# Kernel optimization log

Measured on AMD Instinct MI355X. Metric: run time of the kernel, lower is better.

The kernel has to match this reference:

```python
import jax, jax.numpy as jnp
import numpy as np

SELF_ATTN = -5e4  # reformer TOKEN_SELF_ATTN_VALUE


def _lsh_self_attention(h, w_qk, w_v, w_out, b_out, rotations, n_heads, bucket_size):
    # h: [B, N, D] with N divisible by 2*bucket_size (pre-padded)
    B, N, D = h.shape
    E = D // n_heads
    n_buckets = N // bucket_size
    n_hashes = rotations.shape[1]
    # shared-QK projections, heads merged into batch (batch-major, like reformer)
    qk = (h @ w_qk).reshape(B, N, n_heads, E).transpose(0, 2, 1, 3).reshape(B * n_heads, N, E)
    v = (h @ w_v).reshape(B, N, n_heads, E).transpose(0, 2, 1, 3).reshape(B * n_heads, N, E)
    # --- LSH hashing: argmax over [rot, -rot] ---
    rot = jnp.einsum('bne,ehr->bhnr', qk, rotations)          # [BH, n_hashes, N, n_buckets/2]
    rot = jnp.concatenate([rot, -rot], axis=-1)               # [BH, n_hashes, N, n_buckets]
    buckets = jnp.argmax(rot, axis=-1)                        # [BH, n_hashes, N]
    buckets = buckets + (jnp.arange(n_hashes) * n_buckets)[None, :, None]
    buckets = buckets.reshape(B * n_heads, n_hashes * N)
    # --- sort tokens by (bucket, position) ---
    ticker = jnp.arange(n_hashes * N)
    buckets_and_t = N * buckets + (ticker % N)                # unique keys -> deterministic sort
    sticker = jnp.argsort(buckets_and_t, axis=-1)
    undo = jnp.argsort(sticker, axis=-1)
    st = sticker % N                                          # original positions, sorted order
    sqk = jnp.take_along_axis(qk, st[..., None], axis=1)      # [BH, n_hashes*N, E]
    sv = jnp.take_along_axis(v, st[..., None], axis=1)
    # --- chunk and attend locally (with look-one-back) ---
    nc = n_hashes * n_buckets
    bq = sqk.reshape(-1, nc, bucket_size, E)
    bk = bq / jnp.maximum(jnp.linalg.norm(bq, axis=-1, keepdims=True), 1e-12)  # normalized shared keys
    bv = sv.reshape(-1, nc, bucket_size, E)
    bts = st.reshape(-1, nc, bucket_size)
    look = lambda t: jnp.concatenate([t, jnp.roll(t, 1, axis=1)], axis=2)
    bk, bv, bkt = look(bk), look(bv), look(bts)
    dots = jnp.einsum('bcie,bcje->bcij', bq, bk) * (E ** -0.5)  # [BH, nc, bs, 2*bs]
    dots = jnp.where(bts[..., :, None] == bkt[..., None, :], SELF_ATTN, dots)  # mask self
    lse = jax.scipy.special.logsumexp(dots, axis=-1, keepdims=True)
    p = jnp.exp(dots - lse)
    bo = jnp.einsum('bcij,bcje->bcie', p, bv)
    so = bo.reshape(-1, n_hashes * N, E)
    slog = lse.reshape(-1, n_hashes * N)
    # --- unsort and combine hash rounds by softmax over logsumexp logits ---
    o = jnp.take_along_axis(so, undo[..., None], axis=1).reshape(-1, n_hashes, N, E)
    logits = jnp.take_along_axis(slog, undo, axis=1).reshape(-1, n_hashes, N, 1)
    probs = jnp.exp(logits - jax.scipy.special.logsumexp(logits, axis=1, keepdims=True))
    out = jnp.sum(o * probs, axis=1)                          # [BH, N, E]
    out = out.reshape(B, n_heads, N, E).transpose(0, 2, 1, 3).reshape(B, N, D)
    return out @ w_out + b_out


def setup_inputs() -> dict:
    key = jax.random.key(0)
    ks = jax.random.split(key, 8)
    b, l, n = 16, 12, 325
    d_feat, d_pos, heads, bucket, n_hashes = 256, 64, 8, 16, 4
    pad = 2 * bucket - n % (2 * bucket)
    n_buckets = (n + pad) // bucket
    E = d_feat // heads
    s = 0.05
    return {
        'x': jax.random.normal(ks[0], (b, l, n, d_feat), dtype=jnp.float32),
        'ste': jax.random.normal(ks[1], (b, l, n, d_pos), dtype=jnp.float32),
        'w_proj': jax.random.normal(ks[2], (d_feat + d_pos, d_feat), dtype=jnp.float32) * s,
        'b_proj': jnp.zeros((d_feat,), jnp.float32),
        'w_qk': jax.random.normal(ks[3], (d_feat, d_feat), dtype=jnp.float32) * s,
        'w_v': jax.random.normal(ks[4], (d_feat, d_feat), dtype=jnp.float32) * s,
        'w_out': jax.random.normal(ks[5], (d_feat, d_feat), dtype=jnp.float32) * s,
        'b_out': jnp.zeros((d_feat,), jnp.float32),
        'rotations': jax.random.normal(ks[6], (E, n_hashes, n_buckets // 2), dtype=jnp.float32),
        'n_heads': heads,
        'bucket_size': bucket,
    }


def reference(x, ste, w_proj, b_proj, w_qk, w_v, w_out, b_out, rotations, n_heads, bucket_size):
    b, l, n, d = x.shape
    h = jnp.concatenate([x, ste], axis=-1).reshape(b * l, n, -1)
    h = h @ w_proj + b_proj                                   # projection to d_hidden_feat
    pad = 2 * bucket_size - n % (2 * bucket_size)             # always > 0 (as in the source)
    h = jnp.pad(h, ((0, 0), (0, pad), (0, 0)))
    h = _lsh_self_attention(h, w_qk, w_v, w_out, b_out, rotations, n_heads, bucket_size)
    h = h[:, :-pad, :]
    return h.reshape(b, l, n, -1)
```

## Files before the change

### kernel.cpp

```cpp
#include <hip/hip_runtime.h>
#include <math.h>

#define BL 192
#define NREAL 325
#define NPAD 352
#define DM 256
#define DPOS 64
#define DIN 320
#define NHEADS 8
#define EDIM 32
#define NHASH 4
#define BS 16
#define NBUCK 22
#define NCHUNK 88
#define BHTOT 1536
#define RROT 11
#define W2COLS 352
#define RTM 8
#define HTM 16

__global__ __launch_bounds__(256) void h_kernel(
    const float* __restrict__ x, const float* __restrict__ ste,
    const float* __restrict__ wproj, const float* __restrict__ bproj,
    float* __restrict__ h) {
  int tile = blockIdx.x, bl = blockIdx.y;
  int d = threadIdx.x;
  int n0 = tile * HTM;
  float acc[HTM];
#pragma unroll
  for (int m = 0; m < HTM; ++m) acc[m] = 0.f;
  if (n0 + HTM <= NREAL) {
    const float* xb = x + (size_t)(bl * NREAL + n0) * DM;
    const float* sb = ste + (size_t)(bl * NREAL + n0) * DPOS;
    for (int k = 0; k < DM; k += 4) {
      float b0 = wproj[(k + 0) * DM + d];
      float b1 = wproj[(k + 1) * DM + d];
      float b2 = wproj[(k + 2) * DM + d];
      float b3 = wproj[(k + 3) * DM + d];
#pragma unroll
      for (int m = 0; m < HTM; ++m) {
        const float* xr = xb + (size_t)m * DM + k;
        acc[m] = fmaf(xr[0], b0, acc[m]);
        acc[m] = fmaf(xr[1], b1, acc[m]);
        acc[m] = fmaf(xr[2], b2, acc[m]);
        acc[m] = fmaf(xr[3], b3, acc[m]);
      }
    }
    for (int k = 0; k < DPOS; k += 4) {
      float b0 = wproj[(DM + k + 0) * DM + d];
      float b1 = wproj[(DM + k + 1) * DM + d];
      float b2 = wproj[(DM + k + 2) * DM + d];
      float b3 = wproj[(DM + k + 3) * DM + d];
#pragma unroll
      for (int m = 0; m < HTM; ++m) {
        const float* sr = sb + (size_t)m * DPOS + k;
        acc[m] = fmaf(sr[0], b0, acc[m]);
        acc[m] = fmaf(sr[1], b1, acc[m]);
        acc[m] = fmaf(sr[2], b2, acc[m]);
        acc[m] = fmaf(sr[3], b3, acc[m]);
      }
    }
  } else if (n0 < NREAL) {
#pragma unroll
    for (int m = 0; m < HTM; ++m) {
      if (n0 + m < NREAL) {
        const float* xr = x + (size_t)(bl * NREAL + n0 + m) * DM;
        const float* sr = ste + (size_t)(bl * NREAL + n0 + m) * DPOS;
        for (int k = 0; k < DM; ++k) acc[m] = fmaf(xr[k], wproj[k * DM + d], acc[m]);
        for (int k = 0; k < DPOS; ++k)
          acc[m] = fmaf(sr[k], wproj[(DM + k) * DM + d], acc[m]);
      }
    }
  }
  float bb = bproj[d];
#pragma unroll
  for (int m = 0; m < HTM; ++m) {
    int n = n0 + m;
    h[((size_t)(bl * NPAD + n)) * DM + d] = (n < NREAL) ? (acc[m] + bb) : 0.f;
  }
}

__global__ __launch_bounds__(256) void qkv_rot_bucket_kernel(
    const float* __restrict__ h, const float* __restrict__ wqk,
    const float* __restrict__ wv, const float* __restrict__ rotations,
    int* __restrict__ buckets, float* __restrict__ qk_out,
    float* __restrict__ v_out) {
  int tile = blockIdx.x, bl = blockIdx.y;
  int tid = threadIdx.x;
  __shared__ float Qs[RTM][DM];
  __shared__ float Rs[RTM][W2COLS];
  int n0 = tile * RTM;
  const float* hb = h + (size_t)(bl * NPAD + n0) * DM;
  float aq[RTM], av[RTM];
#pragma unroll
  for (int m = 0; m < RTM; ++m) { aq[m] = 0.f; av[m] = 0.f; }
  for (int k = 0; k < DM; k += 4) {
    float q0 = wqk[(k + 0) * DM + tid];
    float q1 = wqk[(k + 1) * DM + tid];
    float q2 = wqk[(k + 2) * DM + tid];
    float q3 = wqk[(k + 3) * DM + tid];
    float w0 = wv[(k + 0) * DM + tid];
    float w1 = wv[(k + 1) * DM + tid];
    float w2 = wv[(k + 2) * DM + tid];
    float w3 = wv[(k + 3) * DM + tid];
#pragma unroll
    for (int m = 0; m < RTM; ++m) {
      const float* hr = hb + (size_t)m * DM + k;
      float a0 = hr[0], a1 = hr[1], a2 = hr[2], a3 = hr[3];
      aq[m] = fmaf(a0, q0, aq[m]);
      aq[m] = fmaf(a1, q1, aq[m]);
      aq[m] = fmaf(a2, q2, aq[m]);
      aq[m] = fmaf(a3, q3, aq[m]);
      av[m] = fmaf(a0, w0, av[m]);
      av[m] = fmaf(a1, w1, av[m]);
      av[m] = fmaf(a2, w2, av[m]);
      av[m] = fmaf(a3, w3, av[m]);
    }
  }
  {
    int head = tid >> 5, e = tid & 31;
    size_t bh = (size_t)(bl * NHEADS + head);
#pragma unroll
    for (int m = 0; m < RTM; ++m) {
      Qs[m][tid] = aq[m];
      int n = n0 + m;
      qk_out[(bh * NPAD + n) * EDIM + e] = aq[m];
      v_out[(bh * NPAD + n) * EDIM + e] = av[m];
    }
  }
  __syncthreads();
  for (int col = tid; col < W2COLS; col += 256) {
    int head = col / 44;
    int hr = col - head * 44;
    int hs = hr / RROT;
    int r = hr - hs * RROT;
    float acc[RTM];
#pragma unroll
    for (int m = 0; m < RTM; ++m) acc[m] = 0.f;
    {
#pragma clang fp contract(off)
      for (int e = 0; e < EDIM; ++e) {
        float rr = rotations[(e * NHASH + hs) * RROT + r];
#pragma unroll
        for (int m = 0; m < RTM; ++m) {
          float p = Qs[m][head * EDIM + e] * rr;
          acc[m] = acc[m] + p;
        }
      }
    }
#pragma unroll
    for (int m = 0; m < RTM; ++m) Rs[m][col] = acc[m];
  }
  __syncthreads();
  {
    int m = tid >> 5;
    int rest = tid & 31;
    int head = rest >> 2;
    int hs = rest & 3;
    int cbase = head * 44 + hs * RROT;
    float bestv = Rs[m][cbase];
    int best = 0;
    for (int r = 1; r < RROT; ++r) {
      float dv = Rs[m][cbase + r];
      if (dv > bestv) { bestv = dv; best = r; }
    }
    for (int r = 0; r < RROT; ++r) {
      float dv = -Rs[m][cbase + r];
      if (dv > bestv) { bestv = dv; best = RROT + r; }
    }
    int n = n0 + m;
    int bh = bl * NHEADS + head;
    buckets[((size_t)(bh * NHASH + hs)) * NPAD + n] = best;
  }
}

__global__ __launch_bounds__(384) void sort_kernel(const int* __restrict__ buckets,
                                                   int* __restrict__ st) {
  int bh = blockIdx.x, hs = blockIdx.y;
  int n = threadIdx.x;
  __shared__ int buck[NPAD];
  const int* brow = buckets + ((size_t)(bh * NHASH + hs)) * NPAD;
  if (n < NPAD) buck[n] = brow[n];
  __syncthreads();
  if (n < NPAD) {
    int b = buck[n];
    int dest = 0;
    for (int m2 = 0; m2 < NPAD; ++m2) {
      int bm = buck[m2];
      dest += (int)((bm < b) | ((bm == b) & (m2 < n)));
    }
    st[((size_t)(bh * NHASH + hs)) * NPAD + dest] = n;
  }
}

__global__ __launch_bounds__(512) void attn_lse_kernel(
    const float* __restrict__ qk, const int* __restrict__ st,
    float* __restrict__ ll) {
  int c = blockIdx.x, bh = blockIdx.y;
  int t = threadIdx.x;
  int i = t >> 5, j = t & 31;
  __shared__ float qs[16][EDIM];
  __shared__ float ks[32][EDIM + 1];
  __shared__ int qpos[16];
  __shared__ int kpos[32];
  __shared__ float rnorm[32];
  const int* strow = st + (size_t)bh * (NHASH * NPAD);
  int pc = (c + NCHUNK - 1) % NCHUNK;
  if (t < 16) {
    qpos[t] = strow[c * BS + t];
  } else if (t < 48) {
    int jj = t - 16;
    kpos[jj] = (jj < BS) ? strow[c * BS + jj] : strow[pc * BS + (jj - BS)];
  }
  __syncthreads();
  const float* qkb = qk + (size_t)bh * NPAD * EDIM;
  qs[i][j] = qkb[qpos[i] * EDIM + j];
#pragma unroll
  for (int rep = 0; rep < 2; ++rep) {
    int lin = t + rep * 512;
    int r = lin >> 5, cc = lin & 31;
    ks[r][cc] = qkb[kpos[r] * EDIM + cc];
  }
  __syncthreads();
  if (t < 32) {
    float s = 0.f;
#pragma unroll
    for (int e = 0; e < EDIM; ++e) { float kv = ks[t][e]; s = fmaf(kv, kv, s); }
    rnorm[t] = 1.0f / fmaxf(sqrtf(s), 1e-12f);
  }
  __syncthreads();
  float dot = 0.f;
#pragma unroll
  for (int e = 0; e < EDIM; ++e) dot = fmaf(qs[i][e], ks[j][e], dot);
  dot *= rnorm[j] * 0.17677669529663688f;
  if (qpos[i] == kpos[j]) dot = -50000.0f;
  float mx = dot;
#pragma unroll
  for (int off = 16; off > 0; off >>= 1) mx = fmaxf(mx, __shfl_xor(mx, off, 32));
  float ex = expf(dot - mx);
  float sm = ex;
#pragma unroll
  for (int off = 16; off > 0; off >>= 1) sm += __shfl_xor(sm, off, 32);
  if (j == 0) {
    int hs = c / NBUCK;
    ll[((size_t)(bh * NHASH + hs)) * NPAD + qpos[i]] = mx + logf(sm);
  }
}

__global__ __launch_bounds__(256) void lcomb_kernel(const float* __restrict__ ll,
                                                    float* __restrict__ L) {
  int gid = blockIdx.x * 256 + threadIdx.x;
  if (gid >= BHTOT * NPAD) return;
  int n = gid % NPAD, bh = gid / NPAD;
  float l0 = ll[((size_t)(bh * NHASH + 0)) * NPAD + n];
  float l1 = ll[((size_t)(bh * NHASH + 1)) * NPAD + n];
  float l2 = ll[((size_t)(bh * NHASH + 2)) * NPAD + n];
  float l3 = ll[((size_t)(bh * NHASH + 3)) * NPAD + n];
  float m = fmaxf(fmaxf(l0, l1), fmaxf(l2, l3));
  float s = expf(l0 - m) + expf(l1 - m) + expf(l2 - m) + expf(l3 - m);
  L[gid] = m + logf(s);
}

__global__ __launch_bounds__(512) void attn_out_kernel(
    const float* __restrict__ qk, const float* __restrict__ v,
    const int* __restrict__ st, const float* __restrict__ L,
    float* __restrict__ att) {
  int c = blockIdx.x, bh = blockIdx.y;
  int t = threadIdx.x;
  int i = t >> 5, j = t & 31;
  __shared__ float qs[16][EDIM];
  __shared__ float ks[32][EDIM + 1];
  __shared__ float vs[32][EDIM + 1];
  __shared__ float ps[16][32];
  __shared__ int qpos[16];
  __shared__ int kpos[32];
  __shared__ float rnorm[32];
  const int* strow = st + (size_t)bh * (NHASH * NPAD);
  int pc = (c + NCHUNK - 1) % NCHUNK;
  if (t < 16) {
    qpos[t] = strow[c * BS + t];
  } else if (t < 48) {
    int jj = t - 16;
    kpos[jj] = (jj < BS) ? strow[c * BS + jj] : strow[pc * BS + (jj - BS)];
  }
  __syncthreads();
  const float* qkb = qk + (size_t)bh * NPAD * EDIM;
  const float* vb = v + (size_t)bh * NPAD * EDIM;
  qs[i][j] = qkb[qpos[i] * EDIM + j];
#pragma unroll
  for (int rep = 0; rep < 2; ++rep) {
    int lin = t + rep * 512;
    int r = lin >> 5, cc = lin & 31;
    ks[r][cc] = qkb[kpos[r] * EDIM + cc];
    vs[r][cc] = vb[kpos[r] * EDIM + cc];
  }
  __syncthreads();
  if (t < 32) {
    float s = 0.f;
#pragma unroll
    for (int e = 0; e < EDIM; ++e) { float kv = ks[t][e]; s = fmaf(kv, kv, s); }
    rnorm[t] = 1.0f / fmaxf(sqrtf(s), 1e-12f);
  }
  __syncthreads();
  float dot = 0.f;
#pragma unroll
  for (int e = 0; e < EDIM; ++e) dot = fmaf(qs[i][e], ks[j][e], dot);
  dot *= rnorm[j] * 0.17677669529663688f;
  if (qpos[i] == kpos[j]) dot = -50000.0f;
  ps[i][j] = expf(dot - L[(size_t)bh * NPAD + qpos[i]]);
  __syncthreads();
  float acc = 0.f;
#pragma unroll
  for (int jj = 0; jj < 32; ++jj) acc = fmaf(ps[i][jj], vs[jj][j], acc);
  int head = bh & 7, bl = bh >> 3;
  int qp = qpos[i];
  atomicAdd(&att[((size_t)(bl * NPAD + qp)) * DM + head * EDIM + j], acc);
}

__global__ __launch_bounds__(256) void outproj_kernel(
    const float* __restrict__ att, const float* __restrict__ w,
    const float* __restrict__ bias, float* __restrict__ out) {
  int tile = blockIdx.x, bl = blockIdx.y;
  int d = threadIdx.x;
  int n0 = tile * HTM;
  float acc[HTM];
#pragma unroll
  for (int m = 0; m < HTM; ++m) acc[m] = 0.f;
  if (n0 + HTM <= NREAL) {
    const float* ab = att + (size_t)(bl * NPAD + n0) * DM;
    for (int k = 0; k < DM; k += 4) {
      float b0 = w[(k + 0) * DM + d];
      float b1 = w[(k + 1) * DM + d];
      float b2 = w[(k + 2) * DM + d];
      float b3 = w[(k + 3) * DM + d];
#pragma unroll
      for (int m = 0; m < HTM; ++m) {
        const float* ar = ab + (size_t)m * DM + k;
        acc[m] = fmaf(ar[0], b0, acc[m]);
        acc[m] = fmaf(ar[1], b1, acc[m]);
        acc[m] = fmaf(ar[2], b2, acc[m]);
        acc[m] = fmaf(ar[3], b3, acc[m]);
      }
    }
  } else if (n0 < NREAL) {
#pragma unroll
    for (int m = 0; m < HTM; ++m) {
      if (n0 + m < NREAL) {
        const float* ar = att + (size_t)(bl * NPAD + n0 + m) * DM;
        for (int k = 0; k < DM; ++k) acc[m] = fmaf(ar[k], w[k * DM + d], acc[m]);
      }
    }
  } else {
    return;
  }
  float bb = bias[d];
#pragma unroll
  for (int m = 0; m < HTM; ++m) {
    int n = n0 + m;
    if (n < NREAL) out[((size_t)(bl * NREAL + n)) * DM + d] = acc[m] + bb;
  }
}

extern "C" void kernel_launch(void* const* d_in, const int* in_sizes, int n_in,
                              void* d_out, int out_size, void* d_ws, size_t ws_size,
                              hipStream_t stream) {
  (void)in_sizes; (void)n_in; (void)out_size;
  const float* x = (const float*)d_in[0];
  const float* ste = (const float*)d_in[1];
  const float* w_proj = (const float*)d_in[2];
  const float* b_proj = (const float*)d_in[3];
  const float* w_qk = (const float*)d_in[4];
  const float* w_v = (const float*)d_in[5];
  const float* w_out = (const float*)d_in[6];
  const float* b_out = (const float*)d_in[7];
  const float* rotations = (const float*)d_in[8];
  float* out = (float*)d_out;

  const size_t szh = (size_t)BL * NPAD * DM;
  const size_t szst = (size_t)BHTOT * NHASH * NPAD;
  const size_t szL = (size_t)BHTOT * NPAD;
  const size_t needed = 3 * szh * 4 + 2 * szst * 4 + szL * 4;
  if (ws_size < needed) return;

  float* qk = (float*)d_ws;
  float* v = qk + szh;
  float* att = v + szh;
  float* h = att;
  int* st = (int*)(att + szh);
  int* buckets = st + szst;
  float* ll = (float*)buckets;
  float* L = (float*)(buckets + szst);

  h_kernel<<<dim3(NPAD / HTM, BL), dim3(256), 0, stream>>>(
      x, ste, w_proj, b_proj, h);
  qkv_rot_bucket_kernel<<<dim3(NPAD / RTM, BL), dim3(256), 0, stream>>>(
      h, w_qk, w_v, rotations, buckets, qk, v);
  (void)hipMemsetAsync(att, 0, szh * sizeof(float), stream);
  sort_kernel<<<dim3(BHTOT, NHASH), dim3(384), 0, stream>>>(buckets, st);
  attn_lse_kernel<<<dim3(NCHUNK, BHTOT), dim3(512), 0, stream>>>(qk, st, ll);
  lcomb_kernel<<<dim3((BHTOT * NPAD + 255) / 256), dim3(256), 0, stream>>>(ll, L);
  attn_out_kernel<<<dim3(NCHUNK, BHTOT), dim3(512), 0, stream>>>(qk, v, st, L, att);
  outproj_kernel<<<dim3(21, BL), dim3(256), 0, stream>>>(att, w_out, b_out, out);
}
```

Baseline: 1.807 ms.

## Fuse LSH attention LSE, combine and output into one per-head block kernel

Replaces the three attention kernels (per-chunk log-sum-exp, hash combine, output) and the workspace memset with a single kernel that gives each batch-head to one 512-thread block. The block stages all shared-QK rows, key norms and sort indices in LDS once, computes per-hash LSE, combines it across hashes, then recomputes the dots and accumulates outputs into an LDS buffer before writing them out with plain stores. This removes repeated global gathers of q/k/v per chunk, the intermediate ll/L round-trips and the global atomics. In exchange it uses roughly 130KB of LDS per block, which limits occupancy to one block per CU, and it computes the dot products twice.

Result: no change. 1.843 ms (+2.0%).

```diff
diff --git a/kernel.cpp b/kernel.cpp
--- a/kernel.cpp
+++ b/kernel.cpp
@@ -18,6 +18,8 @@
 #define W2COLS 352
 #define RTM 8
 #define HTM 16
+#define QKP 9
+#define OPW 33
 
 __global__ __launch_bounds__(256) void h_kernel(
     const float* __restrict__ x, const float* __restrict__ ste,
@@ -193,128 +195,160 @@
   }
 }
 
-__global__ __launch_bounds__(512) void attn_lse_kernel(
-    const float* __restrict__ qk, const int* __restrict__ st,
-    float* __restrict__ ll) {
-  int c = blockIdx.x, bh = blockIdx.y;
+__global__ __launch_bounds__(512) void attn_fused_kernel(
+    const float* __restrict__ qk, const float* __restrict__ v,
+    const int* __restrict__ st, float* __restrict__ att) {
+  int bh = blockIdx.x;
   int t = threadIdx.x;
-  int i = t >> 5, j = t & 31;
-  __shared__ float qs[16][EDIM];
-  __shared__ float ks[32][EDIM + 1];
-  __shared__ int qpos[16];
-  __shared__ int kpos[32];
-  __shared__ float rnorm[32];
-  const int* strow = st + (size_t)bh * (NHASH * NPAD);
-  int pc = (c + NCHUNK - 1) % NCHUNK;
-  if (t < 16) {
-    qpos[t] = strow[c * BS + t];
-  } else if (t < 48) {
-    int jj = t - 16;
-    kpos[jj] = (jj < BS) ? strow[c * BS + jj] : strow[pc * BS + (jj - BS)];
-  }
-  __syncthreads();
-  const float* qkb = qk + (size_t)bh * NPAD * EDIM;
-  qs[i][j] = qkb[qpos[i] * EDIM + j];
-#pragma unroll
-  for (int rep = 0; rep < 2; ++rep) {
-    int lin = t + rep * 512;
-    int r = lin >> 5, cc = lin & 31;
-    ks[r][cc] = qkb[kpos[r] * EDIM + cc];
-  }
-  __syncthreads();
-  if (t < 32) {
-    float s = 0.f;
-#pragma unroll
-    for (int e = 0; e < EDIM; ++e) { float kv = ks[t][e]; s = fmaf(kv, kv, s); }
-    rnorm[t] = 1.0f / fmaxf(sqrtf(s), 1e-12f);
-  }
-  __syncthreads();
-  float dot = 0.f;
-#pragma unroll
-  for (int e = 0; e < EDIM; ++e) dot = fmaf(qs[i][e], ks[j][e], dot);
-  dot *= rnorm[j] * 0.17677669529663688f;
-  if (qpos[i] == kpos[j]) dot = -50000.0f;
-  float mx = dot;
-#pragma unroll
-  for (int off = 16; off > 0; off >>= 1) mx = fmaxf(mx, __shfl_xor(mx, off, 32));
-  float ex = expf(dot - mx);
-  float sm = ex;
-#pragma unroll
-  for (int off = 16; off > 0; off >>= 1) sm += __shfl_xor(sm, off, 32);
-  if (j == 0) {
-    int hs = c / NBUCK;
-    ll[((size_t)(bh * NHASH + hs)) * NPAD + qpos[i]] = mx + logf(sm);
-  }
-}
-
-__global__ __launch_bounds__(256) void lcomb_kernel(const float* __restrict__ ll,
-                                                    float* __restrict__ L) {
-  int gid = blockIdx.x * 256 + threadIdx.x;
-  if (gid >= BHTOT * NPAD) return;
-  int n = gid % NPAD, bh = gid / NPAD;
-  float l0 = ll[((size_t)(bh * NHASH + 0)) * NPAD + n];
-  float l1 = ll[((size_t)(bh * NHASH + 1)) * NPAD + n];
-  float l2 = ll[((size_t)(bh * NHASH + 2)) * NPAD + n];
-  float l3 = ll[((size_t)(bh * NHASH + 3)) * NPAD + n];
-  float m = fmaxf(fmaxf(l0, l1), fmaxf(l2, l3));
-  float s = expf(l0 - m) + expf(l1 - m) + expf(l2 - m) + expf(l3 - m);
-  L[gid] = m + logf(s);
-}
-
-__global__ __launch_bounds__(512) void attn_out_kernel(
-    const float* __restrict__ qk, const float* __restrict__ v,
-    const int* __restrict__ st, const float* __restrict__ L,
-    float* __restrict__ att) {
-  int c = blockIdx.x, bh = blockIdx.y;
-  int t = threadIdx.x;
-  int i = t >> 5, j = t & 31;
-  __shared__ float qs[16][EDIM];
-  __shared__ float ks[32][EDIM + 1];
-  __shared__ float vs[32][EDIM + 1];
-  __shared__ float ps[16][32];
-  __shared__ int qpos[16];
-  __shared__ int kpos[32];
-  __shared__ float rnorm[32];
-  const int* strow = st + (size_t)bh * (NHASH * NPAD);
-  int pc = (c + NCHUNK - 1) % NCHUNK;
-  if (t < 16) {
-    qpos[t] = strow[c * BS + t];
-  } else if (t < 48) {
-    int jj = t - 16;
-    kpos[jj] = (jj < BS) ? strow[c * BS + jj] : strow[pc * BS + (jj - BS)];
-  }
-  __syncthreads();
+  int w = t >> 6;
+  int lane = t & 63;
+  int i2 = lane >> 5;
+  int j = lane & 31;
+
+  __shared__ float4 qk4[NPAD][QKP];
+  __shared__ float o_s[NPAD * OPW];
+  __shared__ float4 ps4[8][16][QKP];
+  __shared__ float rnorm_s[NPAD];
+  __shared__ int stf[NHASH * NPAD];
+  __shared__ float ll_s[NHASH][NPAD];
+  __shared__ float L_s[NPAD];
+
+  const float* qk_s = (const float*)qk4;
   const float* qkb = qk + (size_t)bh * NPAD * EDIM;
   const float* vb = v + (size_t)bh * NPAD * EDIM;
-  qs[i][j] = qkb[qpos[i] * EDIM + j];
-#pragma unroll
-  for (int rep = 0; rep < 2; ++rep) {
-    int lin = t + rep * 512;
-    int r = lin >> 5, cc = lin & 31;
-    ks[r][cc] = qkb[kpos[r] * EDIM + cc];
-    vs[r][cc] = vb[kpos[r] * EDIM + cc];
-  }
-  __syncthreads();
-  if (t < 32) {
+  const int* strow = st + (size_t)bh * (NHASH * NPAD);
+
+  for (int idx = t; idx < NPAD * 8; idx += 512) {
+    int n = idx >> 3, c4 = idx & 7;
+    qk4[n][c4] = ((const float4*)qkb)[idx];
+  }
+  for (int idx = t; idx < NPAD * OPW; idx += 512) o_s[idx] = 0.f;
+  for (int idx = t; idx < NHASH * NPAD; idx += 512) stf[idx] = strow[idx];
+  __syncthreads();
+  for (int n = t; n < NPAD; n += 512) {
     float s = 0.f;
-#pragma unroll
-    for (int e = 0; e < EDIM; ++e) { float kv = ks[t][e]; s = fmaf(kv, kv, s); }
-    rnorm[t] = 1.0f / fmaxf(sqrtf(s), 1e-12f);
-  }
-  __syncthreads();
-  float dot = 0.f;
-#pragma unroll
-  for (int e = 0; e < EDIM; ++e) dot = fmaf(qs[i][e], ks[j][e], dot);
-  dot *= rnorm[j] * 0.17677669529663688f;
-  if (qpos[i] == kpos[j]) dot = -50000.0f;
-  ps[i][j] = expf(dot - L[(size_t)bh * NPAD + qpos[i]]);
-  __syncthreads();
-  float acc = 0.f;
-#pragma unroll
-  for (int jj = 0; jj < 32; ++jj) acc = fmaf(ps[i][jj], vs[jj][j], acc);
+    for (int e = 0; e < EDIM; ++e) {
+      float kv = qk_s[n * 36 + e];
+      s = fmaf(kv, kv, s);
+    }
+    rnorm_s[n] = 1.0f / fmaxf(sqrtf(s), 1e-12f);
+  }
+  __syncthreads();
+
+  for (int c = w; c < NCHUNK; c += 8) {
+    int pc = (c + NCHUNK - 1) % NCHUNK;
+    int hs = c / NBUCK;
+    int kp = (j < BS) ? stf[c * BS + j] : stf[pc * BS + (j - BS)];
+    float kr[EDIM];
+    {
+      const float4* krow = qk4[kp];
+#pragma unroll
+      for (int e4 = 0; e4 < 8; ++e4) {
+        float4 kv = krow[e4];
+        kr[e4 * 4 + 0] = kv.x; kr[e4 * 4 + 1] = kv.y;
+        kr[e4 * 4 + 2] = kv.z; kr[e4 * 4 + 3] = kv.w;
+      }
+    }
+    float scale = rnorm_s[kp] * 0.17677669529663688f;
+#pragma unroll
+    for (int i = 0; i < 8; ++i) {
+      int q = i * 2 + i2;
+      int qp = stf[c * BS + q];
+      const float4* qrow = qk4[qp];
+      float dot = 0.f;
+#pragma unroll
+      for (int e4 = 0; e4 < 8; ++e4) {
+        float4 qv = qrow[e4];
+        dot = fmaf(qv.x, kr[e4 * 4 + 0], dot);
+        dot = fmaf(qv.y, kr[e4 * 4 + 1], dot);
+        dot = fmaf(qv.z, kr[e4 * 4 + 2], dot);
+        dot = fmaf(qv.w, kr[e4 * 4 + 3], dot);
+      }
+      dot *= scale;
+      if (qp == kp) dot = -50000.0f;
+      float mx = dot;
+#pragma unroll
+      for (int off = 16; off > 0; off >>= 1) mx = fmaxf(mx, __shfl_xor(mx, off, 32));
+      float ex = expf(dot - mx);
+      float sm = ex;
+#pragma unroll
+      for (int off = 16; off > 0; off >>= 1) sm += __shfl_xor(sm, off, 32);
+      if (j == 0) ll_s[hs][qp] = mx + logf(sm);
+    }
+  }
+  __syncthreads();
+  for (int n = t; n < NPAD; n += 512) {
+    float l0 = ll_s[0][n], l1 = ll_s[1][n], l2 = ll_s[2][n], l3 = ll_s[3][n];
+    float m = fmaxf(fmaxf(l0, l1), fmaxf(l2, l3));
+    float s = expf(l0 - m) + expf(l1 - m) + expf(l2 - m) + expf(l3 - m);
+    L_s[n] = m + logf(s);
+  }
+  __syncthreads();
+
+  float* psw = (float*)ps4[w];
+  for (int c = w; c < NCHUNK; c += 8) {
+    int pc = (c + NCHUNK - 1) % NCHUNK;
+    int kp = (j < BS) ? stf[c * BS + j] : stf[pc * BS + (j - BS)];
+    float kr[EDIM];
+    {
+      const float4* krow = qk4[kp];
+#pragma unroll
+      for (int e4 = 0; e4 < 8; ++e4) {
+        float4 kv = krow[e4];
+        kr[e4 * 4 + 0] = kv.x; kr[e4 * 4 + 1] = kv.y;
+        kr[e4 * 4 + 2] = kv.z; kr[e4 * 4 + 3] = kv.w;
+      }
+    }
+    float scale = rnorm_s[kp] * 0.17677669529663688f;
+#pragma unroll
+    for (int i = 0; i < 8; ++i) {
+      int q = i * 2 + i2;
+      int qp = stf[c * BS + q];
+      const float4* qrow = qk4[qp];
+      float dot = 0.f;
+#pragma unroll
+      for (int e4 = 0; e4 < 8; ++e4) {
+        float4 qv = qrow[e4];
+        dot = fmaf(qv.x, kr[e4 * 4 + 0], dot);
+        dot = fmaf(qv.y, kr[e4 * 4 + 1], dot);
+        dot = fmaf(qv.z, kr[e4 * 4 + 2], dot);
+        dot = fmaf(qv.w, kr[e4 * 4 + 3], dot);
+      }
+      dot *= scale;
+      if (qp == kp) dot = -50000.0f;
+      psw[q * 36 + j] = expf(dot - L_s[qp]);
+    }
+    __syncthreads();
+    float vr[32];
+#pragma unroll
+    for (int jj = 0; jj < 32; ++jj) {
+      int kpj = (jj < BS) ? stf[c * BS + jj] : stf[pc * BS + (jj - BS)];
+      vr[jj] = vb[kpj * EDIM + j];
+    }
+#pragma unroll
+    for (int i = 0; i < 8; ++i) {
+      int q = i * 2 + i2;
+      int qp = stf[c * BS + q];
+      const float4* prow = (const float4*)(psw + q * 36);
+      float acc = 0.f;
+#pragma unroll
+      for (int j4 = 0; j4 < 8; ++j4) {
+        float4 pv = prow[j4];
+        acc = fmaf(pv.x, vr[j4 * 4 + 0], acc);
+        acc = fmaf(pv.y, vr[j4 * 4 + 1], acc);
+        acc = fmaf(pv.z, vr[j4 * 4 + 2], acc);
+        acc = fmaf(pv.w, vr[j4 * 4 + 3], acc);
+      }
+      atomicAdd(&o_s[qp * OPW + j], acc);
+    }
+  }
+  __syncthreads();
   int head = bh & 7, bl = bh >> 3;
-  int qp = qpos[i];
-  atomicAdd(&att[((size_t)(bl * NPAD + qp)) * DM + head * EDIM + j], acc);
+  float* attb = att + ((size_t)bl * NPAD) * DM + head * EDIM;
+  for (int idx = t; idx < NPAD * EDIM; idx += 512) {
+    int n = idx >> 5, e = idx & 31;
+    attb[(size_t)n * DM + e] = o_s[n * OPW + e];
+  }
 }
 
 __global__ __launch_bounds__(256) void outproj_kernel(
@@ -378,8 +412,7 @@
 
   const size_t szh = (size_t)BL * NPAD * DM;
   const size_t szst = (size_t)BHTOT * NHASH * NPAD;
-  const size_t szL = (size_t)BHTOT * NPAD;
-  const size_t needed = 3 * szh * 4 + 2 * szst * 4 + szL * 4;
+  const size_t needed = 3 * szh * 4 + 2 * szst * 4;
   if (ws_size < needed) return;
 
   float* qk = (float*)d_ws;
@@ -388,17 +421,12 @@
   float* h = att;
   int* st = (int*)(att + szh);
   int* buckets = st + szst;
-  float* ll = (float*)buckets;
-  float* L = (float*)(buckets + szst);
 
   h_kernel<<<dim3(NPAD / HTM, BL), dim3(256), 0, stream>>>(
       x, ste, w_proj, b_proj, h);
   qkv_rot_bucket_kernel<<<dim3(NPAD / RTM, BL), dim3(256), 0, stream>>>(
       h, w_qk, w_v, rotations, buckets, qk, v);
-  (void)hipMemsetAsync(att, 0, szh * sizeof(float), stream);
   sort_kernel<<<dim3(BHTOT, NHASH), dim3(384), 0, stream>>>(buckets, st);
-  attn_lse_kernel<<<dim3(NCHUNK, BHTOT), dim3(512), 0, stream>>>(qk, st, ll);
-  lcomb_kernel<<<dim3((BHTOT * NPAD + 255) / 256), dim3(256), 0, stream>>>(ll, L);
-  attn_out_kernel<<<dim3(NCHUNK, BHTOT), dim3(512), 0, stream>>>(qk, v, st, L, att);
+  attn_fused_kernel<<<dim3(BHTOT), dim3(512), 0, stream>>>(qk, v, st, att);
   outproj_kernel<<<dim3(21, BL), dim3(256), 0, stream>>>(att, w_out, b_out, out);
 }
```
